# Kernel optimization log

Hardware: AMD Instinct MI355X
Metric: run time of the kernel (lower is better)

Reference implementation:

```python
import jax, jax.numpy as jnp
import numpy as np

B, S, HID, NH, AH, F = 1024, 100, 128, 2, 64, 2
DH = HID // NH          # item/pos head size = 64
DA = AH // NH           # attribute head size = 32
EPS = 1e-12


def setup_inputs() -> dict:
    key = jax.random.key(0)
    ks = iter(jax.random.split(key, 32))
    n = lambda shape, s=0.02: jax.random.normal(next(ks), shape, dtype=jnp.float32) * s
    inp = {
        "input_tensor": jax.random.normal(next(ks), (B, S, HID), dtype=jnp.float32),
        "attribute_table": jax.random.normal(next(ks), (F, B, S, AH), dtype=jnp.float32),
        "position_embedding": jax.random.normal(next(ks), (B, S, HID), dtype=jnp.float32),
        "attention_mask": jnp.zeros((B, 1, S, S), dtype=jnp.float32),
        # item / positional projections (stored [in, out])
        "Wq": n((HID, HID)), "bq": jnp.zeros((HID,), jnp.float32),
        "Wk": n((HID, HID)), "bk": jnp.zeros((HID,), jnp.float32),
        "Wv": n((HID, HID)), "bv": jnp.zeros((HID,), jnp.float32),
        "Wqp": n((HID, HID)), "bqp": jnp.zeros((HID,), jnp.float32),
        "Wkp": n((HID, HID)), "bkp": jnp.zeros((HID,), jnp.float32),
        # per-attribute projections, stacked over feat axis
        "Wq_attr": n((F, AH, AH)), "bq_attr": jnp.zeros((F, AH), jnp.float32),
        "Wk_attr": n((F, AH, AH)), "bk_attr": jnp.zeros((F, AH), jnp.float32),
        # gate fusion (VanillaAttentionX): Linear(S,S) -> ReLU -> Linear(S,1)
        "fuse_W1": n((S, S)), "fuse_b1": jnp.zeros((S,), jnp.float32),
        "fuse_W2": n((S, 1)), "fuse_b2": jnp.zeros((1,), jnp.float32),
        # output dense + LayerNorm
        "Wd": n((HID, HID)), "bd": jnp.zeros((HID,), jnp.float32),
        "ln_g": jnp.ones((HID,), jnp.float32), "ln_b": jnp.zeros((HID,), jnp.float32),
    }
    return inp


def _split_heads(x, nh):  # [B,S,nh*d] -> [B,nh,S,d]
    b, s, hd = x.shape
    return x.reshape(b, s, nh, hd // nh).transpose(0, 2, 1, 3)


def reference(input_tensor, attribute_table, position_embedding, attention_mask,
              Wq, bq, Wk, bk, Wv, bv, Wqp, bqp, Wkp, bkp,
              Wq_attr, bq_attr, Wk_attr, bk_attr,
              fuse_W1, fuse_b1, fuse_W2, fuse_b2,
              Wd, bd, ln_g, ln_b):
    b, s, hid = input_tensor.shape
    # item / positional QKV
    q = _split_heads(input_tensor @ Wq + bq, NH)
    k = _split_heads(input_tensor @ Wk + bk, NH)
    v = _split_heads(input_tensor @ Wv + bv, NH)
    qp = _split_heads(position_embedding @ Wqp + bqp, NH)
    kp = _split_heads(position_embedding @ Wkp + bkp, NH)
    item_scores = jnp.einsum('bhqd,bhkd->bhqk', q, k)
    pos_scores = jnp.einsum('bhqd,bhkd->bhqk', qp, kp)
    # attribute score streams: [F,B,S,AH] -> [F,B,NH,S,DA]
    aq = jnp.einsum('fbsa,fao->fbso', attribute_table, Wq_attr) + bq_attr[:, None, None, :]
    ak = jnp.einsum('fbsa,fao->fbso', attribute_table, Wk_attr) + bk_attr[:, None, None, :]
    aq = aq.reshape(F, b, s, NH, DA).transpose(0, 1, 3, 2, 4)
    ak = ak.reshape(F, b, s, NH, DA).transpose(0, 1, 3, 2, 4)
    attr_scores = jnp.einsum('fbhqd,fbhkd->fbhqk', aq, ak)  # [F,B,NH,S,S]
    # gate fusion: stack streams on axis -2 -> [B,NH,S,F+2,S]
    stacked = jnp.concatenate([
        jnp.moveaxis(attr_scores, 0, 3),
        item_scores[:, :, :, None, :],
        pos_scores[:, :, :, None, :],
    ], axis=-2)
    energy = jax.nn.relu(stacked @ fuse_W1 + fuse_b1) @ fuse_W2 + fuse_b2  # [B,NH,S,F+2,1]
    gate_w = jax.nn.softmax(energy[..., 0], axis=-1)                       # [B,NH,S,F+2]
    fused = jnp.einsum('bhsfk,bhsf->bhsk', stacked, gate_w)                # [B,NH,S,S]
    scores = fused / jnp.sqrt(jnp.asarray(DH, fused.dtype)) + attention_mask
    probs = jax.nn.softmax(scores, axis=-1)
    ctx = jnp.einsum('bhqk,bhkd->bhqd', probs, v)
    ctx = ctx.transpose(0, 2, 1, 3).reshape(b, s, hid)
    h = ctx @ Wd + bd + input_tensor
    mu = jnp.mean(h, axis=-1, keepdims=True)
    var = jnp.mean((h - mu) ** 2, axis=-1, keepdims=True)
    return (h - mu) / jnp.sqrt(var + EPS) * ln_g + ln_b
```

## Files before the change

### kernel.cpp

```cpp
#include <hip/hip_runtime.h>
#include <hip/hip_bf16.h>

using bf16 = __hip_bfloat16;
using u16 = unsigned short;
typedef __attribute__((ext_vector_type(8))) short bf16x8;
typedef __attribute__((ext_vector_type(16))) float f32x16;

namespace {

constexpr int B_  = 1024;
constexpr int Sd  = 100;
constexpr int BS_ = B_ * Sd;

constexpr int NTHR = 1024;
constexpr int NW   = 16;

constexpr int STP = 420;
constexpr int STS = 104;
constexpr int QKP = 196;
constexpr int AP  = 132;
constexpr int ATP = 68;
constexpr int W1P = 116;
constexpr int VTP = 116;

constexpr int O_ST = 0;
constexpr int O_Q  = 84000;
constexpr int O_K  = 123200;
constexpr int E2S  = 32000;
constexpr int LBYTES = 162400;

constexpr int WQT_E  = 0;
constexpr int WKT_E  = 16384;
constexpr int WQPT_E = 32768;
constexpr int WKPT_E = 49152;
constexpr int WVT_E  = 65536;
constexpr int WAT_E  = 81920;
constexpr int W1T_E  = 98304;
constexpr int WDT_E  = 113152;
constexpr size_t WS_NEED = 129536ull * 2;

__device__ __forceinline__ float bfr(u16 u) {
  unsigned int x = ((unsigned int)u) << 16;
  float f; __builtin_memcpy(&f, &x, 4); return f;
}
__device__ __forceinline__ u16 f2bu(float x) {
  bf16 h = __float2bfloat16(x);
  u16 u; __builtin_memcpy(&u, &h, 2); return u;
}
__device__ __forceinline__ float4 ld4(const float* p) {
  return *reinterpret_cast<const float4*>(p);
}
__device__ __forceinline__ float wsum(float v) {
#pragma unroll
  for (int m = 32; m > 0; m >>= 1) v += __shfl_xor(v, m);
  return v;
}
__device__ __forceinline__ float wmax(float v) {
#pragma unroll
  for (int m = 32; m > 0; m >>= 1) v = fmaxf(v, __shfl_xor(v, m));
  return v;
}
__device__ __forceinline__ f32x16 zf16() {
  f32x16 z;
#pragma unroll
  for (int i = 0; i < 16; ++i) z[i] = 0.f;
  return z;
}
__device__ __forceinline__ f32x16 MFMA32(bf16x8 a, bf16x8 b, f32x16 c) {
  return __builtin_amdgcn_mfma_f32_32x32x16_bf16(a, b, c, 0, 0, 0);
}

__device__ __forceinline__ bf16x8 ld8(const u16* p) {
  const ushort4 a = *reinterpret_cast<const ushort4*>(p);
  const ushort4 b = *reinterpret_cast<const ushort4*>(p + 4);
  bf16x8 f;
  f[0] = (short)a.x; f[1] = (short)a.y; f[2] = (short)a.z; f[3] = (short)a.w;
  f[4] = (short)b.x; f[5] = (short)b.y; f[6] = (short)b.z; f[7] = (short)b.w;
  return f;
}

template <int L4>
__device__ __forceinline__ void stage_rows4(const float* __restrict__ src, u16* dst,
                                            int nrow, int pitch, int tid, int nthr) {
  for (int i = tid; i < (nrow << L4); i += nthr) {
    const int rr = i >> L4, cc = (i & ((1 << L4) - 1)) << 2;
    const float4 v = *reinterpret_cast<const float4*>(src + ((size_t)rr << (L4 + 2)) + cc);
    ushort4 o;
    o.x = f2bu(v.x); o.y = f2bu(v.y); o.z = f2bu(v.z); o.w = f2bu(v.w);
    *reinterpret_cast<ushort4*>(dst + rr * pitch + cc) = o;
  }
}
template <int LC>
__device__ __forceinline__ void stage_wt(const float* __restrict__ W, int ldw, int coff,
                                         u16* dst, int kd, int pitch, int tid, int nthr) {
  constexpr int NC = 1 << LC;
  for (int idx = tid; idx < NC * kd; idx += nthr) {
    const int k = idx >> LC, c = idx & (NC - 1);
    dst[c * pitch + k] = f2bu(W[k * ldw + coff + c]);
  }
}
__device__ __forceinline__ void stage_wt6(const float* __restrict__ W, int coff,
                                          u16* dst, int tid, int nthr) {
  stage_wt<6>(W, 128, coff, dst, 128, AP, tid, nthr);
}
__device__ __forceinline__ void copy_w64(const u16* __restrict__ src, u16* dst,
                                         int tid, int nthr) {
  for (int i = tid; i < 2048; i += nthr) {
    const int r = i >> 5, c4 = (i & 31) << 2;
    *reinterpret_cast<ushort4*>(dst + r * AP + c4) =
        *reinterpret_cast<const ushort4*>(src + r * 128 + c4);
  }
}

template <int KD, bool TR>
__device__ __forceinline__ void tile32(const u16* A, int apitch, const u16* Wt, int wpitch,
                                       const float* __restrict__ bias, u16* dst, int dpitch,
                                       int dbase, int m0, int n0, int l) {
  const int cr = l & 31, g = l >> 5;
  int ar = m0 + cr; if (ar >= Sd) ar = Sd - 1;
  const u16* ap = A + ar * apitch + g * 8;
  const u16* bp = Wt + (n0 + cr) * wpitch + g * 8;
  f32x16 acc = zf16();
#pragma unroll
  for (int k0 = 0; k0 < KD; k0 += 16)
    acc = MFMA32(ld8(ap + k0), ld8(bp + k0), acc);
  const float bvv = bias[n0 + cr];
#pragma unroll
  for (int i = 0; i < 16; ++i) {
    const int row = m0 + (i & 3) + 8 * (i >> 2) + 4 * g;
    if (row < Sd) {
      if (TR) dst[(n0 + cr) * dpitch + dbase + row] = f2bu(acc[i] + bvv);
      else    dst[row * dpitch + dbase + n0 + cr]   = f2bu(acc[i] + bvv);
    }
  }
}

__global__ __launch_bounds__(256) void prep_weights(
    const float* __restrict__ Wq, const float* __restrict__ Wk,
    const float* __restrict__ Wqp, const float* __restrict__ Wkp,
    const float* __restrict__ Wv, const float* __restrict__ Wqa,
    const float* __restrict__ Wka, const float* __restrict__ W1,
    const float* __restrict__ Wd, u16* __restrict__ ws) {
  const int t = blockIdx.x * 256 + threadIdx.x;
  const int NT = gridDim.x * 256;
  const float* srcs[5] = {Wq, Wk, Wqp, Wkp, Wv};
#pragma unroll
  for (int wsel = 0; wsel < 5; ++wsel) {
    u16* dst = ws + wsel * 16384;
    const float* src = srcs[wsel];
    for (int i = t; i < 16384; i += NT) {
      const int h = i >> 13, c = (i >> 7) & 63, k = i & 127;
      dst[i] = f2bu(src[k * 128 + h * 64 + c]);
    }
  }
  for (int i = t; i < 16384; i += NT) {
    const int pr = i >> 12, h = (i >> 11) & 1, c = (i >> 6) & 31, k = i & 63;
    const float* src = (pr & 1) ? Wka : Wqa;
    ws[WAT_E + i] = f2bu(src[(pr >> 1) * 4096 + k * 64 + h * 32 + c]);
  }
  for (int i = t; i < 14848; i += NT) {
    const int c = i / W1P, k = i - c * W1P;
    ws[W1T_E + i] = (c < Sd && k < Sd) ? f2bu(W1[k * Sd + c]) : (u16)0;
  }
  for (int i = t; i < 16384; i += NT) {
    const int c = i >> 7, k = i & 127;
    ws[WDT_E + i] = f2bu(Wd[k * 128 + c]);
  }
}

template <bool PREP>
__global__ __launch_bounds__(NTHR) void attn_mega(
    const float* __restrict__ input, const float* __restrict__ attrT,
    const float* __restrict__ posE, const float* __restrict__ mask,
    const float* __restrict__ Wq, const float* __restrict__ bq,
    const float* __restrict__ Wk, const float* __restrict__ bk,
    const float* __restrict__ Wv, const float* __restrict__ bv,
    const float* __restrict__ Wqp, const float* __restrict__ bqp,
    const float* __restrict__ Wkp, const float* __restrict__ bkp,
    const float* __restrict__ Wqa, const float* __restrict__ bqa,
    const float* __restrict__ Wka, const float* __restrict__ bka,
    const float* __restrict__ W1, const float* __restrict__ b1,
    const float* __restrict__ W2, const u16* __restrict__ wsw,
    float* __restrict__ ctx) {
  __shared__ __align__(16) char L[LBYTES];
  u16* const ST = (u16*)(L + O_ST);
  u16* const QC = (u16*)(L + O_Q);
  u16* const KC = (u16*)(L + O_K);
  u16* const SA  = (u16*)(L + O_ST);
  u16* const SW1 = (u16*)(L + O_ST + 26400);
  u16* const SW2 = (u16*)(L + O_ST + 43296);
  u16* const AT0  = (u16*)(L + O_ST);
  u16* const AT1  = (u16*)(L + O_ST + 13600);
  u16* const WA0Q = (u16*)(L + O_ST + 27200);
  u16* const WA0K = (u16*)(L + O_ST + 31552);
  u16* const WA1Q = (u16*)(L + O_ST + 35904);
  u16* const WA1K = (u16*)(L + O_ST + 40256);
  u16* const W1T = (u16*)(L + O_K);
  float* const e2s = (float*)(L + O_K + E2S);
  u16* const VA  = (u16*)(L + O_Q);
  u16* const WVT = (u16*)(L + O_K);
  u16* const VT  = (u16*)(L + O_K + 16896);

  const int tid = threadIdx.x;
  const int bh = blockIdx.x;
  const int b = bh >> 1, h = bh & 1;
  const size_t row0 = (size_t)b * Sd;
  const int l = tid & 63, w = tid >> 6;
  const int cr = l & 31, g = l >> 5;

  stage_rows4<5>(input + row0 * 128, SA, 100, AP, tid, NTHR);
  if constexpr (PREP) {
    copy_w64(wsw + WQT_E + h * 8192, SW1, tid, NTHR);
    copy_w64(wsw + WKT_E + h * 8192, SW2, tid, NTHR);
  } else {
    stage_wt6(Wq, h * 64, SW1, tid, NTHR);
    stage_wt6(Wk, h * 64, SW2, tid, NTHR);
  }
  float4 r2[8];
#pragma unroll
  for (int s = 0; s < 8; ++s) {
    if (PREP && s >= 4) break;
    const int fi = tid + s * NTHR;
    if (fi < 3200) {
      r2[s] = ld4(posE + row0 * 128 + fi * 4);
    } else if (!PREP && fi < 5248) {
      const int f2 = fi - 3200, k = f2 >> 4, c0 = (f2 & 15) << 2;
      r2[s] = ld4(Wqp + k * 128 + h * 64 + c0);
    } else if (!PREP && fi < 7296) {
      const int f2 = fi - 5248, k = f2 >> 4, c0 = (f2 & 15) << 2;
      r2[s] = ld4(Wkp + k * 128 + h * 64 + c0);
    }
  }
  __syncthreads();

  {
    const int pr = w >> 3, mt = (w >> 1) & 3, nt = w & 1;
    tile32<128, false>(SA, AP, pr ? SW2 : SW1, AP, (pr ? bk : bq) + h * 64,
                       pr ? KC : QC, QKP, 0, mt * 32, nt * 32, l);
  }
  __syncthreads();

#pragma unroll
  for (int s = 0; s < 8; ++s) {
    if (PREP && s >= 4) break;
    const int fi = tid + s * NTHR;
    if (fi < 3200) {
      ushort4 o;
      o.x = f2bu(r2[s].x); o.y = f2bu(r2[s].y); o.z = f2bu(r2[s].z); o.w = f2bu(r2[s].w);
      *reinterpret_cast<ushort4*>(SA + (fi >> 5) * AP + ((fi & 31) << 2)) = o;
    } else if (!PREP && fi < 5248) {
      const int f2 = fi - 3200, k = f2 >> 4, c0 = (f2 & 15) << 2;
      SW1[c0 * AP + k] = f2bu(r2[s].x); SW1[(c0 + 1) * AP + k] = f2bu(r2[s].y);
      SW1[(c0 + 2) * AP + k] = f2bu(r2[s].z); SW1[(c0 + 3) * AP + k] = f2bu(r2[s].w);
    } else if (!PREP && fi < 7296) {
      const int f2 = fi - 5248, k = f2 >> 4, c0 = (f2 & 15) << 2;
      SW2[c0 * AP + k] = f2bu(r2[s].x); SW2[(c0 + 1) * AP + k] = f2bu(r2[s].y);
      SW2[(c0 + 2) * AP + k] = f2bu(r2[s].z); SW2[(c0 + 3) * AP + k] = f2bu(r2[s].w);
    }
  }
  if constexpr (PREP) {
    copy_w64(wsw + WQPT_E + h * 8192, SW1, tid, NTHR);
    copy_w64(wsw + WKPT_E + h * 8192, SW2, tid, NTHR);
  }
  float4 r3[6];
#pragma unroll
  for (int s = 0; s < 6; ++s) {
    if (PREP && s >= 4) break;
    const int fi = tid + s * NTHR;
    if (fi < 1600) {
      r3[s] = ld4(attrT + (size_t)b * 6400 + fi * 4);
    } else if (fi < 3200) {
      r3[s] = ld4(attrT + (size_t)(B_ + b) * 6400 + (fi - 1600) * 4);
    } else if (!PREP && fi < 5248) {
      const int f3 = fi - 3200, which = f3 >> 9, fj = f3 & 511;
      const int k = fj >> 3, c0 = (fj & 7) << 2;
      const float* src = (which == 0) ? Wqa : (which == 1) ? Wka
                       : (which == 2) ? (Wqa + 4096) : (Wka + 4096);
      r3[s] = ld4(src + k * 64 + h * 32 + c0);
    }
  }
  __syncthreads();

  {
    const int pr = w >> 3, mt = (w >> 1) & 3, nt = w & 1;
    tile32<128, false>(SA, AP, pr ? SW2 : SW1, AP, (pr ? bkp : bqp) + h * 64,
                       pr ? KC : QC, QKP, 64, mt * 32, nt * 32, l);
  }
  __syncthreads();

#pragma unroll
  for (int s = 0; s < 6; ++s) {
    if (PREP && s >= 4) break;
    const int fi = tid + s * NTHR;
    if (fi < 1600) {
      ushort4 o;
      o.x = f2bu(r3[s].x); o.y = f2bu(r3[s].y); o.z = f2bu(r3[s].z); o.w = f2bu(r3[s].w);
      *reinterpret_cast<ushort4*>(AT0 + (fi >> 4) * ATP + ((fi & 15) << 2)) = o;
    } else if (fi < 3200) {
      const int f3 = fi - 1600;
      ushort4 o;
      o.x = f2bu(r3[s].x); o.y = f2bu(r3[s].y); o.z = f2bu(r3[s].z); o.w = f2bu(r3[s].w);
      *reinterpret_cast<ushort4*>(AT1 + (f3 >> 4) * ATP + ((f3 & 15) << 2)) = o;
    } else if (!PREP && fi < 5248) {
      const int f3 = fi - 3200, which = f3 >> 9, fj = f3 & 511;
      const int k = fj >> 3, c0 = (fj & 7) << 2;
      u16* dst = (which == 0) ? WA0Q : (which == 1) ? WA0K
               : (which == 2) ? WA1Q : WA1K;
      dst[c0 * ATP + k] = f2bu(r3[s].x); dst[(c0 + 1) * ATP + k] = f2bu(r3[s].y);
      dst[(c0 + 2) * ATP + k] = f2bu(r3[s].z); dst[(c0 + 3) * ATP + k] = f2bu(r3[s].w);
    }
  }
  if constexpr (PREP) {
    for (int i = tid; i < 2048; i += NTHR) {
      const int pr = i >> 9, row = (i >> 4) & 31, c4 = (i & 15) << 2;
      u16* dst = (pr == 0) ? WA0Q : (pr == 1) ? WA0K : (pr == 2) ? WA1Q : WA1K;
      *reinterpret_cast<ushort4*>(dst + row * ATP + c4) =
          *reinterpret_cast<const ushort4*>(wsw + WAT_E + pr * 4096 + h * 2048 + row * 64 + c4);
    }
  }
  float4 r5[3];
  ushort4 rw1[4];
  if constexpr (PREP) {
#pragma unroll
    for (int s = 0; s < 4; ++s) {
      const int fi = tid + s * NTHR;
      if (fi < 3712) rw1[s] = reinterpret_cast<const ushort4*>(wsw + W1T_E)[fi];
    }
  } else {
#pragma unroll
    for (int s = 0; s < 3; ++s) {
      const int fi = tid + s * NTHR;
      if (fi < 2500) r5[s] = ld4(W1 + fi * 4);
    }
  }
  __syncthreads();

  {
    const int pr = w >> 2, mt = w & 3;
    const u16* Asrc = (pr < 2) ? AT0 : AT1;
    const u16* Wt = (pr == 0) ? WA0Q : (pr == 1) ? WA0K : (pr == 2) ? WA1Q : WA1K;
    const float* bs = (pr == 0) ? bqa + h * 32 : (pr == 1) ? bka + h * 32
                     : (pr == 2) ? bqa + 64 + h * 32 : bka + 64 + h * 32;
    tile32<64, false>(Asrc, ATP, Wt, ATP, bs, (pr & 1) ? KC : QC, QKP,
                      128 + (pr >> 1) * 32, mt * 32, 0, l);
  }
  __syncthreads();

  {
    ushort4 z; z.x = z.y = z.z = z.w = 0;
    for (int q = tid; q < Sd; q += NTHR)
      *reinterpret_cast<ushort4*>(ST + q * STP + 416) = z;
  }
  {
    const int mt = w >> 2, nt = w & 3;
    const int m0 = mt * 32, n0 = nt * 32;
    int ar = m0 + cr; if (ar >= Sd) ar = Sd - 1;
    int br = n0 + cr; if (br >= Sd) br = Sd - 1;
    const u16* ap = QC + ar * QKP + g * 8;
    const u16* bp = KC + br * QKP + g * 8;
    f32x16 ai = zf16(), po = zf16(), a0 = zf16(), a1 = zf16();
    ai = MFMA32(ld8(ap + 0),   ld8(bp + 0),   ai);
    ai = MFMA32(ld8(ap + 16),  ld8(bp + 16),  ai);
    ai = MFMA32(ld8(ap + 32),  ld8(bp + 32),  ai);
    ai = MFMA32(ld8(ap + 48),  ld8(bp + 48),  ai);
    po = MFMA32(ld8(ap + 64),  ld8(bp + 64),  po);
    po = MFMA32(ld8(ap + 80),  ld8(bp + 80),  po);
    po = MFMA32(ld8(ap + 96),  ld8(bp + 96),  po);
    po = MFMA32(ld8(ap + 112), ld8(bp + 112), po);
    a0 = MFMA32(ld8(ap + 128), ld8(bp + 128), a0);
    a0 = MFMA32(ld8(ap + 144), ld8(bp + 144), a0);
    a1 = MFMA32(ld8(ap + 160), ld8(bp + 160), a1);
    a1 = MFMA32(ld8(ap + 176), ld8(bp + 176), a1);
    const int col = n0 + cr;
    if (col < STS) {
#pragma unroll
      for (int i = 0; i < 16; ++i) {
        const int row = m0 + (i & 3) + 8 * (i >> 2) + 4 * g;
        if (row < Sd) {
          u16* sp = ST + row * STP + col;
          sp[0]       = f2bu(a0[i]);
          sp[STS]     = f2bu(a1[i]);
          sp[2 * STS] = f2bu(ai[i]);
          sp[3 * STS] = f2bu(po[i]);
        }
      }
    }
  }
  __syncthreads();

  if constexpr (PREP) {
#pragma unroll
    for (int s = 0; s < 4; ++s) {
      const int fi = tid + s * NTHR;
      if (fi < 3712) reinterpret_cast<ushort4*>(W1T)[fi] = rw1[s];
    }
  } else {
    {
      ushort4 z; z.x = z.y = z.z = z.w = 0;
      if (tid < 812)
        *reinterpret_cast<ushort4*>(W1T + 11600 + tid * 4) = z;
      if (tid < 400) {
        const int c = tid >> 2, kq = 100 + ((tid & 3) << 2);
        *reinterpret_cast<ushort4*>(W1T + c * W1P + kq) = z;
      }
    }
#pragma unroll
    for (int s = 0; s < 3; ++s) {
      const int fi = tid + s * NTHR;
      if (fi < 2500) {
#pragma unroll
        for (int j = 0; j < 4; ++j) {
          const int o = fi * 4 + j;
          const int k = o / 100, c = o - k * 100;
          W1T[c * W1P + k] = f2bu((j == 0) ? r5[s].x : (j == 1) ? r5[s].y
                                  : (j == 2) ? r5[s].z : r5[s].w);
        }
      }
    }
  }
  if (tid < 8) ((u16*)(L + O_Q))[tid] = 0;
  __syncthreads();

  {
    float b1v[4], w2v[4];
#pragma unroll
    for (int nt = 0; nt < 4; ++nt) {
      const int c = nt * 32 + cr;
      b1v[nt] = (c < Sd) ? b1[c] : 0.f;
      w2v[nt] = (c < Sd) ? W2[c] : 0.f;
    }
    for (int mt = w; mt < 13; mt += NW) {
      const int m0 = mt * 32;
      int gr = m0 + cr; if (gr > 399) gr = 399;
      const u16* ap = ST + (gr >> 2) * STP + (gr & 3) * STS + g * 8;
      f32x16 c0 = zf16(), c1 = zf16(), c2 = zf16(), c3 = zf16();
#pragma unroll
      for (int k0 = 0; k0 < 112; k0 += 16) {
        const bf16x8 af = ld8(ap + k0);
        c0 = MFMA32(af, ld8(W1T + (cr)      * W1P + g * 8 + k0), c0);
        c1 = MFMA32(af, ld8(W1T + (32 + cr) * W1P + g * 8 + k0), c1);
        c2 = MFMA32(af, ld8(W1T + (64 + cr) * W1P + g * 8 + k0), c2);
        c3 = MFMA32(af, ld8(W1T + (96 + cr) * W1P + g * 8 + k0), c3);
      }
#pragma unroll
      for (int i = 0; i < 16; ++i) {
        float v = fmaxf(c0[i] + b1v[0], 0.f) * w2v[0]
                + fmaxf(c1[i] + b1v[1], 0.f) * w2v[1]
                + fmaxf(c2[i] + b1v[2], 0.f) * w2v[2]
                + fmaxf(c3[i] + b1v[3], 0.f) * w2v[3];
#pragma unroll
        for (int mm = 1; mm < 32; mm <<= 1) v += __shfl_xor(v, mm);
        if (cr == 0) {
          const int go = m0 + (i & 3) + 8 * (i >> 2) + 4 * g;
          if (go < 400) e2s[go] = v;
        }
      }
    }
  }
  __syncthreads();

  if (w >= 8) {
    const int t2 = tid - 512;
    stage_rows4<5>(input + row0 * 128, VA, 100, AP, t2, 512);
    if constexpr (PREP) {
      copy_w64(wsw + WVT_E + h * 8192, WVT, t2, 512);
    } else {
      stage_wt6(Wv, h * 64, WVT, t2, 512);
    }
    ushort4 z; z.x = z.y = z.z = z.w = 0;
    for (int i2 = t2; i2 < 64 * VTP / 4; i2 += 512)
      *reinterpret_cast<ushort4*>(VT + i2 * 4) = z;
  } else {
    for (int q = w; q < Sd; q += 8) {
      const float* ez = e2s + q * 4;
      float e0 = ez[0], e1 = ez[1], e2v = ez[2], e3 = ez[3];
      const float mg = fmaxf(fmaxf(e0, e1), fmaxf(e2v, e3));
      e0 = __expf(e0 - mg); e1 = __expf(e1 - mg);
      e2v = __expf(e2v - mg); e3 = __expf(e3 - mg);
      const float ginv = 1.0f / (e0 + e1 + e2v + e3);
      const float g0v = e0 * ginv, g1v = e1 * ginv, g2v = e2v * ginv, g3v = e3 * ginv;
      u16* const sp = ST + q * STP;
      const float* const mp = mask + (size_t)b * 10000 + q * 100;
      float x1 = g0v * bfr(sp[l]) + g1v * bfr(sp[STS + l]) +
                 g2v * bfr(sp[2 * STS + l]) + g3v * bfr(sp[3 * STS + l]);
      x1 = x1 * 0.125f + mp[l];
      const bool v2 = (l < 36);
      float x2 = -3e38f;
      if (v2) {
        const int k2 = 64 + l;
        x2 = g0v * bfr(sp[k2]) + g1v * bfr(sp[STS + k2]) +
             g2v * bfr(sp[2 * STS + k2]) + g3v * bfr(sp[3 * STS + k2]);
        x2 = x2 * 0.125f + mp[k2];
      }
      const float M = wmax(fmaxf(x1, x2));
      const float ea = __expf(x1 - M);
      const float eb = v2 ? __expf(x2 - M) : 0.f;
      const float inv = 1.0f / wsum(ea + eb);
      sp[l] = f2bu(ea * inv);
      if (v2) sp[64 + l] = f2bu(eb * inv);
    }
  }
  __syncthreads();

  if (w < 8) {
    const int mt = w >> 1, nt = w & 1;
    tile32<128, true>(VA, AP, WVT, AP, bv + h * 64, VT, VTP, 0, mt * 32, nt * 32, l);
  }
  __syncthreads();

  if (w < 8) {
    const int mt = w >> 1, nt = w & 1;
    const int m0 = mt * 32, n0 = nt * 32;
    int ar = m0 + cr; if (ar >= Sd) ar = Sd - 1;
    const u16* ap = ST + ar * STP + g * 8;
    const u16* bp = VT + (n0 + cr) * VTP + g * 8;
    f32x16 acc = zf16();
#pragma unroll
    for (int k0 = 0; k0 < 112; k0 += 16)
      acc = MFMA32(ld8(ap + k0), ld8(bp + k0), acc);
#pragma unroll
    for (int i = 0; i < 16; ++i) {
      const int row = m0 + (i & 3) + 8 * (i >> 2) + 4 * g;
      if (row < Sd)
        ctx[(row0 + row) * 128 + h * 64 + n0 + cr] = acc[i];
    }
  }
}

template <bool PREP>
__global__ __launch_bounds__(512) void dense_ln(
    const float* __restrict__ ctxg, const float* __restrict__ Wd,
    const float* __restrict__ bd, const float* __restrict__ resid,
    const float* __restrict__ lng, const float* __restrict__ lnb,
    const u16* __restrict__ wsw, float* __restrict__ out) {
  __shared__ __align__(16) char L[101376];
  u16* const Ab  = (u16*)L;
  u16* const WdT = (u16*)(L + 33792);
  u16* const Hs  = (u16*)(L + 67584);
  const int tid = threadIdx.x;
  const size_t row0 = (size_t)blockIdx.x * 128;
  const int l = tid & 63, w = tid >> 6, cr = l & 31, g = l >> 5;

  stage_rows4<5>(ctxg + row0 * 128, Ab, 128, AP, tid, 512);
  if constexpr (PREP) {
    for (int i = tid; i < 4096; i += 512) {
      const int r = i >> 5, c4 = (i & 31) << 2;
      *reinterpret_cast<ushort4*>(WdT + r * AP + c4) =
          *reinterpret_cast<const ushort4*>(wsw + WDT_E + r * 128 + c4);
    }
  } else {
    stage_wt<7>(Wd, 128, 0, WdT, 128, AP, tid, 512);
  }
  __syncthreads();

  for (int u = w; u < 16; u += 8) {
    const int m0 = (u >> 2) * 32, n0 = (u & 3) * 32;
    const u16* ap = Ab + (m0 + cr) * AP + g * 8;
    const u16* bp = WdT + (n0 + cr) * AP + g * 8;
    f32x16 acc = zf16();
#pragma unroll
    for (int k0 = 0; k0 < 128; k0 += 16)
      acc = MFMA32(ld8(ap + k0), ld8(bp + k0), acc);
#pragma unroll
    for (int i = 0; i < 16; ++i) {
      const int row = m0 + (i & 3) + 8 * (i >> 2) + 4 * g;
      Hs[row * AP + n0 + cr] = f2bu(acc[i]);
    }
  }
  __syncthreads();

  for (int rr = w; rr < 128; rr += 8) {
    const size_t grow = row0 + rr;
    const float h1 = bfr(Hs[rr * AP + l])      + bd[l]      + resid[grow * 128 + l];
    const float h2 = bfr(Hs[rr * AP + 64 + l]) + bd[64 + l] + resid[grow * 128 + 64 + l];
    const float mu = wsum(h1 + h2) * (1.0f / 128.0f);
    const float d1 = h1 - mu, d2 = h2 - mu;
    const float var = wsum(d1 * d1 + d2 * d2) * (1.0f / 128.0f);
    const float rs = rsqrtf(var + 1e-12f);
    out[grow * 128 + l]      = d1 * rs * lng[l]      + lnb[l];
    out[grow * 128 + 64 + l] = d2 * rs * lng[64 + l] + lnb[64 + l];
  }
}

}

extern "C" void kernel_launch(void* const* d_in, const int* in_sizes, int n_in,
                              void* d_out, int out_size, void* d_ws,
                              size_t ws_size, hipStream_t stream) {
  (void)in_sizes; (void)n_in; (void)out_size;

  const float* input = (const float*)d_in[0];
  const float* attrT = (const float*)d_in[1];
  const float* posE  = (const float*)d_in[2];
  const float* mask  = (const float*)d_in[3];
  const float* Wq  = (const float*)d_in[4];  const float* bq  = (const float*)d_in[5];
  const float* Wk  = (const float*)d_in[6];  const float* bk  = (const float*)d_in[7];
  const float* Wv  = (const float*)d_in[8];  const float* bv  = (const float*)d_in[9];
  const float* Wqp = (const float*)d_in[10]; const float* bqp = (const float*)d_in[11];
  const float* Wkp = (const float*)d_in[12]; const float* bkp = (const float*)d_in[13];
  const float* Wqa = (const float*)d_in[14]; const float* bqa = (const float*)d_in[15];
  const float* Wka = (const float*)d_in[16]; const float* bka = (const float*)d_in[17];
  const float* W1  = (const float*)d_in[18]; const float* b1  = (const float*)d_in[19];
  const float* W2  = (const float*)d_in[20];
  const float* Wd  = (const float*)d_in[22]; const float* bd  = (const float*)d_in[23];
  const float* lng = (const float*)d_in[24]; const float* lnb = (const float*)d_in[25];

  float* ctx = (float*)d_out;

  if (ws_size >= WS_NEED) {
    u16* wsw = (u16*)d_ws;
    prep_weights<<<dim3(128), dim3(256), 0, stream>>>(
        Wq, Wk, Wqp, Wkp, Wv, Wqa, Wka, W1, Wd, wsw);
    attn_mega<true><<<dim3(B_ * 2), dim3(NTHR), 0, stream>>>(
        input, attrT, posE, mask, Wq, bq, Wk, bk, Wv, bv, Wqp, bqp, Wkp, bkp,
        Wqa, bqa, Wka, bka, W1, b1, W2, wsw, ctx);
    dense_ln<true><<<dim3(BS_ / 128), dim3(512), 0, stream>>>(
        ctx, Wd, bd, input, lng, lnb, wsw, ctx);
  } else {
    attn_mega<false><<<dim3(B_ * 2), dim3(NTHR), 0, stream>>>(
        input, attrT, posE, mask, Wq, bq, Wk, bk, Wv, bv, Wqp, bqp, Wkp, bkp,
        Wqa, bqa, Wka, bka, W1, b1, W2, nullptr, ctx);
    dense_ln<false><<<dim3(BS_ / 128), dim3(512), 0, stream>>>(
        ctx, Wd, bd, input, lng, lnb, nullptr, ctx);
  }
}
```

Before: 355.3 us.

## Spread V staging and gate softmax across all warps with register-prefetched loads

The phase where 8 warps staged the input rows and Wv while the other 8 ran the gate/softmax now has all 16 warps do both. Global loads for the input rows, Wv and the mask rows are issued into registers first, so their latency overlaps the softmax math; the values are then converted and written to shared memory. This removes the imbalance between the two warp groups and hides global-load latency, at the cost of more registers per thread (about 16 floats for input, 14 for mask), which could cut occupancy or cause spills.

```diff
diff --git a/kernel.cpp b/kernel.cpp
--- a/kernel.cpp
+++ b/kernel.cpp
@@ -459,45 +459,83 @@
   }
   __syncthreads();
 
-  if (w >= 8) {
-    const int t2 = tid - 512;
-    stage_rows4<5>(input + row0 * 128, VA, 100, AP, t2, 512);
+  {
+    float4 va[4];
+#pragma unroll
+    for (int s = 0; s < 4; ++s) {
+      const int fi = tid + s * NTHR;
+      if (fi < 3200) va[s] = ld4(input + row0 * 128 + fi * 4);
+    }
+    ushort4 wv[2];
     if constexpr (PREP) {
-      copy_w64(wsw + WVT_E + h * 8192, WVT, t2, 512);
+#pragma unroll
+      for (int s = 0; s < 2; ++s)
+        wv[s] = reinterpret_cast<const ushort4*>(wsw + WVT_E + h * 8192)[tid + s * NTHR];
+    }
+    float m1r[7], m2r[7];
+#pragma unroll
+    for (int it = 0; it < 7; ++it) {
+      const int q = w + it * NW;
+      if (q < Sd) {
+        const float* mp = mask + (size_t)b * 10000 + q * 100;
+        m1r[it] = mp[l];
+        m2r[it] = (l < 36) ? mp[64 + l] : 0.f;
+      }
+    }
+    {
+      ushort4 z; z.x = z.y = z.z = z.w = 0;
+      for (int i2 = tid; i2 < 64 * VTP / 4; i2 += NTHR)
+        *reinterpret_cast<ushort4*>(VT + i2 * 4) = z;
+    }
+#pragma unroll
+    for (int it = 0; it < 7; ++it) {
+      const int q = w + it * NW;
+      if (q < Sd) {
+        const float* ez = e2s + q * 4;
+        float e0 = ez[0], e1 = ez[1], e2v = ez[2], e3 = ez[3];
+        const float mg = fmaxf(fmaxf(e0, e1), fmaxf(e2v, e3));
+        e0 = __expf(e0 - mg); e1 = __expf(e1 - mg);
+        e2v = __expf(e2v - mg); e3 = __expf(e3 - mg);
+        const float ginv = 1.0f / (e0 + e1 + e2v + e3);
+        const float g0v = e0 * ginv, g1v = e1 * ginv, g2v = e2v * ginv, g3v = e3 * ginv;
+        u16* const sp = ST + q * STP;
+        float x1 = g0v * bfr(sp[l]) + g1v * bfr(sp[STS + l]) +
+                   g2v * bfr(sp[2 * STS + l]) + g3v * bfr(sp[3 * STS + l]);
+        x1 = x1 * 0.125f + m1r[it];
+        const bool v2 = (l < 36);
+        float x2 = -3e38f;
+        if (v2) {
+          const int k2 = 64 + l;
+          x2 = g0v * bfr(sp[k2]) + g1v * bfr(sp[STS + k2]) +
+               g2v * bfr(sp[2 * STS + k2]) + g3v * bfr(sp[3 * STS + k2]);
+          x2 = x2 * 0.125f + m2r[it];
+        }
+        const float M = wmax(fmaxf(x1, x2));
+        const float ea = __expf(x1 - M);
+        const float eb = v2 ? __expf(x2 - M) : 0.f;
+        const float inv = 1.0f / wsum(ea + eb);
+        sp[l] = f2bu(ea * inv);
+        if (v2) sp[64 + l] = f2bu(eb * inv);
+      }
+    }
+#pragma unroll
+    for (int s = 0; s < 4; ++s) {
+      const int fi = tid + s * NTHR;
+      if (fi < 3200) {
+        ushort4 o;
+        o.x = f2bu(va[s].x); o.y = f2bu(va[s].y); o.z = f2bu(va[s].z); o.w = f2bu(va[s].w);
+        *reinterpret_cast<ushort4*>(VA + (fi >> 5) * AP + ((fi & 31) << 2)) = o;
+      }
+    }
+    if constexpr (PREP) {
+#pragma unroll
+      for (int s = 0; s < 2; ++s) {
+        const int i2 = tid + s * NTHR;
+        const int r = i2 >> 5, c4 = (i2 & 31) << 2;
+        *reinterpret_cast<ushort4*>(WVT + r * AP + c4) = wv[s];
+      }
     } else {
-      stage_wt6(Wv, h * 64, WVT, t2, 512);
-    }
-    ushort4 z; z.x = z.y = z.z = z.w = 0;
-    for (int i2 = t2; i2 < 64 * VTP / 4; i2 += 512)
-      *reinterpret_cast<ushort4*>(VT + i2 * 4) = z;
-  } else {
-    for (int q = w; q < Sd; q += 8) {
-      const float* ez = e2s + q * 4;
-      float e0 = ez[0], e1 = ez[1], e2v = ez[2], e3 = ez[3];
-      const float mg = fmaxf(fmaxf(e0, e1), fmaxf(e2v, e3));
-      e0 = __expf(e0 - mg); e1 = __expf(e1 - mg);
-      e2v = __expf(e2v - mg); e3 = __expf(e3 - mg);
-      const float ginv = 1.0f / (e0 + e1 + e2v + e3);
-      const float g0v = e0 * ginv, g1v = e1 * ginv, g2v = e2v * ginv, g3v = e3 * ginv;
-      u16* const sp = ST + q * STP;
-      const float* const mp = mask + (size_t)b * 10000 + q * 100;
-      float x1 = g0v * bfr(sp[l]) + g1v * bfr(sp[STS + l]) +
-                 g2v * bfr(sp[2 * STS + l]) + g3v * bfr(sp[3 * STS + l]);
-      x1 = x1 * 0.125f + mp[l];
-      const bool v2 = (l < 36);
-      float x2 = -3e38f;
-      if (v2) {
-        const int k2 = 64 + l;
-        x2 = g0v * bfr(sp[k2]) + g1v * bfr(sp[STS + k2]) +
-             g2v * bfr(sp[2 * STS + k2]) + g3v * bfr(sp[3 * STS + k2]);
-        x2 = x2 * 0.125f + mp[k2];
-      }
-      const float M = wmax(fmaxf(x1, x2));
-      const float ea = __expf(x1 - M);
-      const float eb = v2 ? __expf(x2 - M) : 0.f;
-      const float inv = 1.0f / wsum(ea + eb);
-      sp[l] = f2bu(ea * inv);
-      if (v2) sp[64 + l] = f2bu(eb * inv);
+      stage_wt6(Wv, h * 64, WVT, tid, NTHR);
     }
   }
   __syncthreads();
```

Result: faster. 318.3 us (-10.4%).
